# Kernel optimization log

Hardware: AMD Instinct MI355X
Metric: run time of the kernel (lower is better)

## Reference

```python
import jax, jax.numpy as jnp
import numpy as np

B, T, C = 8, 2048, 1024
H, D = 16, 64
DLOW = 64  # D_DECAY = D_AAA = D_MV = D_GATE = 64
EPS_LN = 1e-5


def setup_inputs() -> dict:
    key = jax.random.key(0)
    ks = jax.random.split(key, 26)
    p = lambda k, shape, s=0.02: (jax.random.normal(k, shape, jnp.float32) * s)
    u = lambda k, shape: jax.random.uniform(k, shape, jnp.float32)
    return {
        "x":   jax.random.normal(ks[0], (B, T, C), jnp.float32),
        # token-shift mix coefficients (1,1,C)
        "x_r": u(ks[1], (1, 1, C)), "x_w": u(ks[2], (1, 1, C)),
        "x_k": u(ks[3], (1, 1, C)), "x_v": u(ks[4], (1, 1, C)),
        "x_a": u(ks[5], (1, 1, C)), "x_g": u(ks[6], (1, 1, C)),
        # decay lora: w1 [C,DLOW], w2 [DLOW,H], w0 [1,1,H,1]
        "w0": p(ks[7], (1, 1, H, 1)), "w1": p(ks[8], (C, DLOW)), "w2": p(ks[9], (DLOW, H)),
        # in-context lr lora
        "a0": p(ks[10], (1, 1, H, 1)), "a1": p(ks[11], (C, DLOW)), "a2": p(ks[12], (DLOW, H)),
        # value residual lora
        "v0": p(ks[13], (1, 1, C)), "v1": p(ks[14], (C, DLOW)), "v2": p(ks[15], (DLOW, C)),
        # gate lora
        "g1": p(ks[16], (C, DLOW)), "g2": p(ks[17], (DLOW, C)),
        "k_k": 0.85 + p(ks[18], (1, 1, C)),
        "r_k": p(ks[19], (H, D)),
        # main projections, stored [in, out] so x @ W matches nn.Linear
        "Wr": p(ks[20], (C, C)), "Wk": p(ks[21], (C, C)),
        "Wv": p(ks[22], (C, C)), "Wo": p(ks[23], (C, C)),
        # GroupNorm(n_head, n_embd) affine params
        "ln_w": jnp.ones((C,), jnp.float32) + p(ks[24], (C,)),
        "ln_b": p(ks[25], (C,)),
    }


def reference(x, x_r, x_w, x_k, x_v, x_a, x_g,
              w0, w1, w2, a0, a1, a2, v0, v1, v2, g1, g2,
              k_k, r_k, Wr, Wk, Wv, Wo, ln_w, ln_b):
    Bb, Tt, Cc = x.shape
    Hh, Dd = r_k.shape
    # token shift: sx = x_t - x_{t-1} (zero-padded)
    xx = jnp.concatenate([jnp.zeros((Bb, 1, Cc), x.dtype), x[:, :-1]], axis=1)
    sx = x - xx
    xr = x + sx * x_r
    xw = x + sx * x_w
    xk = x + sx * x_k
    xv = x + sx * x_v
    xa = x + sx * x_a
    xg = x + sx * x_g

    r = (xr @ Wr).reshape(Bb, Tt, Hh, Dd)
    # decay in (0, exp(-0.5)): exp(-softplus(-(w0 + lora)) - 0.5)
    w = jnp.exp(-jax.nn.softplus(-(w0 + (jnp.tanh(xw @ w1) @ w2).reshape(Bb, Tt, Hh, 1))) - 0.5)
    k = xk @ Wk
    v = xv @ Wv
    v_res_gate = jax.nn.sigmoid(v0 + jnp.tanh(xv @ v1) @ v2)
    v = v + (v - v) * v_res_gate  # no-op, kept for faithfulness
    a = jax.nn.sigmoid(a0 + (jnp.tanh(xa @ a1) @ a2).reshape(Bb, Tt, Hh, 1))
    g = jax.nn.sigmoid(jnp.tanh(xg @ g1) @ g2)

    kk = (k * k_k).reshape(Bb, Tt, Hh, Dd)
    kk = kk / jnp.maximum(jnp.linalg.norm(kk, axis=-1, keepdims=True), 1e-12)
    vh = v.reshape(Bb, Tt, Hh, Dd)

    # WKV linear recurrence: state = state * w_t + kk_t * v_t * a_t
    kv = (kk * vh * a).astype(jnp.float32)            # [B,T,H,D]
    w_t = jnp.moveaxis(w.astype(jnp.float32), 1, 0)   # [T,B,H,1]
    kv_t = jnp.moveaxis(kv, 1, 0)                     # [T,B,H,D]

    def step(state, inputs):
        wt, kvt = inputs
        state = state * wt + kvt
        return state, state

    init = jnp.zeros((Bb, Hh, Dd), jnp.float32)
    _, states = jax.lax.scan(step, init, (w_t, kv_t))  # [T,B,H,D]
    x_wkv = jnp.moveaxis(states, 0, 1).astype(x.dtype)  # [B,T,H,D]

    x_wkv = x_wkv * r
    bonus = jnp.sum(r * kk * r_k, axis=-1, keepdims=True) * vh
    x_wkv = x_wkv + bonus  # [B,T,H,D]

    # GroupNorm(H groups over C channels), per (B*T) sample
    mean = x_wkv.mean(axis=-1, keepdims=True)
    var = x_wkv.var(axis=-1, keepdims=True)
    xn = (x_wkv - mean) * jax.lax.rsqrt(var + EPS_LN)
    xn = xn.reshape(Bb, Tt, Cc) * ln_w + ln_b

    return (xn * g) @ Wo
```

## Files before the change

kernel.cpp:

```cpp
#include <hip/hip_runtime.h>


typedef __bf16 bf16;
typedef __attribute__((ext_vector_type(8))) __bf16 bf16x8;
typedef __attribute__((ext_vector_type(4))) float f32x4;

#define TBTOK 16384
#define TSEQ  2048
#define CDIM  1024
#define HN    16
#define CHUNK 32
#define NCH   64

__device__ __forceinline__ float wredsum(float v) {
#pragma unroll
  for (int o = 32; o > 0; o >>= 1) v += __shfl_xor(v, o, 64);
  return v;
}
__device__ __forceinline__ float redsum8(float v) {
#pragma unroll
  for (int o = 4; o > 0; o >>= 1) v += __shfl_xor(v, o, 64);
  return v;
}
__device__ __forceinline__ float sigmf(float x) { return 1.f / (1.f + expf(-x)); }

__device__ __forceinline__ void gl_lds16(const bf16* g, bf16* l) {
  __builtin_amdgcn_global_load_lds(
      (const __attribute__((address_space(1))) unsigned int*)g,
      (__attribute__((address_space(3))) unsigned int*)l, 16, 0, 0);
}

__global__ __launch_bounds__(256) void prep_kern(
    const float* __restrict__ x, const float* __restrict__ mr,
    const float* __restrict__ mk, const float* __restrict__ mv,
    bf16* __restrict__ xr, bf16* __restrict__ xk, bf16* __restrict__ xv,
    bf16* __restrict__ xbf,
    const float* __restrict__ Wr, const float* __restrict__ Wk,
    const float* __restrict__ Wv, const float* __restrict__ Wo,
    const float* __restrict__ w1, const float* __restrict__ a1, const float* __restrict__ g1,
    const float* __restrict__ mw, const float* __restrict__ ma, const float* __restrict__ mg,
    const float* __restrict__ g2, const float* __restrict__ w2, const float* __restrict__ a2,
    bf16* __restrict__ WrT, bf16* __restrict__ WkT, bf16* __restrict__ WvT, bf16* __restrict__ WoT,
    bf16* __restrict__ Bcat, bf16* __restrict__ g2T,
    bf16* __restrict__ w2T, bf16* __restrict__ a2T, float* __restrict__ zpad) {
  int bid0 = blockIdx.x;
  int tid = threadIdx.x;
  if (bid0 < 8192) {
    long i8 = ((long)bid0 * 256 + tid) * 8;
    int m = (int)(i8 >> 10);
    int c = (int)(i8 & 1023);
    f32x4 x0 = *(const f32x4*)(x + i8);
    f32x4 x1 = *(const f32x4*)(x + i8 + 4);
    f32x4 p0 = {0.f, 0.f, 0.f, 0.f}, p1 = {0.f, 0.f, 0.f, 0.f};
    if ((m & (TSEQ - 1)) != 0) {
      p0 = *(const f32x4*)(x + i8 - CDIM);
      p1 = *(const f32x4*)(x + i8 - CDIM + 4);
    }
    f32x4 r0 = *(const f32x4*)(mr + c), r1 = *(const f32x4*)(mr + c + 4);
    f32x4 k0 = *(const f32x4*)(mk + c), k1 = *(const f32x4*)(mk + c + 4);
    f32x4 v0 = *(const f32x4*)(mv + c), v1 = *(const f32x4*)(mv + c + 4);
    bf16x8 or_, ok_, ov_, ox_;
#pragma unroll
    for (int j = 0; j < 4; j++) {
      float s0 = x0[j] - p0[j], s1 = x1[j] - p1[j];
      or_[j] = (bf16)(x0[j] + s0 * r0[j]); or_[4 + j] = (bf16)(x1[j] + s1 * r1[j]);
      ok_[j] = (bf16)(x0[j] + s0 * k0[j]); ok_[4 + j] = (bf16)(x1[j] + s1 * k1[j]);
      ov_[j] = (bf16)(x0[j] + s0 * v0[j]); ov_[4 + j] = (bf16)(x1[j] + s1 * v1[j]);
      ox_[j] = (bf16)x0[j];                ox_[4 + j] = (bf16)x1[j];
    }
    *(bf16x8*)(xr + i8) = or_;
    *(bf16x8*)(xk + i8) = ok_;
    *(bf16x8*)(xv + i8) = ov_;
    *(bf16x8*)(xbf + i8) = ox_;
    return;
  }
  int bid = bid0 - 8192;
  int tx = tid & 31, ty = tid >> 5;
  __shared__ bf16 tile[32][33];
  if (bid < 4096) {
    int sel = bid >> 10, t = bid & 1023;
    int k0 = (t >> 5) * 32, n0 = (t & 31) * 32;
    const float* src = sel == 0 ? Wr : (sel == 1 ? Wk : (sel == 2 ? Wv : Wo));
    bf16* dst = sel == 0 ? WrT : (sel == 1 ? WkT : (sel == 2 ? WvT : WoT));
#pragma unroll
    for (int i = 0; i < 4; i++)
      tile[ty + i * 8][tx] = (bf16)src[(long)(k0 + ty + i * 8) * 1024 + n0 + tx];
    __syncthreads();
#pragma unroll
    for (int i = 0; i < 4; i++)
      dst[(long)(n0 + ty + i * 8) * 1024 + k0 + tx] = tile[tx][ty + i * 8];
  } else if (bid < 4480) {
    int idx = bid - 4096;
    int mat = idx >> 7, rem = idx & 127;
    int half = rem >> 6, t = rem & 63;
    int k0 = (t >> 1) * 32, n0 = (t & 1) * 32;
    const float* W = mat == 0 ? w1 : (mat == 1 ? a1 : g1);
    const float* mx = mat == 0 ? mw : (mat == 1 ? ma : mg);
#pragma unroll
    for (int i = 0; i < 4; i++) {
      int k = k0 + ty + i * 8;
      float s = half == 0 ? (1.f + mx[k]) : (-mx[k]);
      tile[ty + i * 8][tx] = (bf16)(s * W[(long)k * 64 + n0 + tx]);
    }
    __syncthreads();
#pragma unroll
    for (int i = 0; i < 4; i++)
      Bcat[(long)(mat * 64 + n0 + ty + i * 8) * 2048 + half * 1024 + k0 + tx] =
          tile[tx][ty + i * 8];
  } else if (bid < 4544) {
    int t = bid - 4480;
    int k0 = (t >> 5) * 32, n0 = (t & 31) * 32;
#pragma unroll
    for (int i = 0; i < 4; i++)
      tile[ty + i * 8][tx] = (bf16)g2[(long)(k0 + ty + i * 8) * 1024 + n0 + tx];
    __syncthreads();
#pragma unroll
    for (int i = 0; i < 4; i++)
      g2T[(long)(n0 + ty + i * 8) * 64 + k0 + tx] = tile[tx][ty + i * 8];
  } else {
#pragma unroll
    for (int rep = 0; rep < 4; rep++) {
      int idx = rep * 256 + tid;
      int k = idx >> 4, h = idx & 15;
      w2T[h * 64 + k] = (bf16)w2[idx];
      a2T[h * 64 + k] = (bf16)a2[idx];
    }
    if (tid < 64) zpad[tid] = 0.f;
  }
}

template <int ACT, typename OT>
__global__ __launch_bounds__(256) void gemm128_kern(
    const bf16* __restrict__ A0, const bf16* __restrict__ A1, const bf16* __restrict__ A2,
    int apitch,
    const bf16* __restrict__ BT0, const bf16* __restrict__ BT1, const bf16* __restrict__ BT2,
    OT* __restrict__ out0, OT* __restrict__ out1, OT* __restrict__ out2,
    int opitch, int K, int nbpm) {
  int bx = blockIdx.x;
  int mat = bx / nbpm;
  int ncol0 = (bx % nbpm) * 128;
  const bf16* Am = mat == 0 ? A0 : (mat == 1 ? A1 : A2);
  const bf16* BTm = mat == 0 ? BT0 : (mat == 1 ? BT1 : BT2);
  OT* out = mat == 0 ? out0 : (mat == 1 ? out1 : out2);
  int m0 = blockIdx.y * 128;

  __shared__ bf16 Al[128 * 64];
  __shared__ bf16 Bl[128 * 64];

  int tid = threadIdx.x;
  int w = tid >> 6, lane = tid & 63, quad = lane >> 4, lr = lane & 15;
  int wm = (w & 1) * 64, wn = (w >> 1) * 64;

  f32x4 acc[4][4] = {};

  int r0 = tid >> 3;
  int slot = tid & 7;
  int kg = (slot ^ (r0 & 7)) * 8;
  const bf16* ag = Am + (long)(m0 + r0) * apitch + kg;
  const bf16* bg = BTm + (long)(ncol0 + r0) * K + kg;
  long astep = (long)32 * apitch;
  long bstep = (long)32 * K;
  bf16* la = Al + w * 512;
  bf16* lb = Bl + w * 512;

  for (int k0 = 0; k0 < K; k0 += 64) {
#pragma unroll
    for (int s = 0; s < 4; s++) gl_lds16(ag + s * astep, la + s * 2048);
#pragma unroll
    for (int s = 0; s < 4; s++) gl_lds16(bg + s * bstep, lb + s * 2048);
    ag += 64; bg += 64;
    __syncthreads();
#pragma unroll
    for (int ko = 0; ko < 2; ko++) {
      bf16x8 af[4], bff[4];
#pragma unroll
      for (int i = 0; i < 4; i++) {
        int ra = wm + i * 16 + lr;
        af[i] = *(const bf16x8*)&Al[ra * 64 + (((ko * 4 + quad) ^ (ra & 7)) * 8)];
      }
#pragma unroll
      for (int j = 0; j < 4; j++) {
        int rb = wn + j * 16 + lr;
        bff[j] = *(const bf16x8*)&Bl[rb * 64 + (((ko * 4 + quad) ^ (rb & 7)) * 8)];
      }
#pragma unroll
      for (int i = 0; i < 4; i++)
#pragma unroll
        for (int j = 0; j < 4; j++)
          acc[i][j] = __builtin_amdgcn_mfma_f32_16x16x32_bf16(af[i], bff[j], acc[i][j], 0, 0, 0);
    }
    __syncthreads();
  }
#pragma unroll
  for (int i = 0; i < 4; i++)
#pragma unroll
    for (int j = 0; j < 4; j++)
#pragma unroll
      for (int rg = 0; rg < 4; rg++) {
        int row = m0 + wm + i * 16 + quad * 4 + rg;
        int col = ncol0 + wn + j * 16 + lr;
        float v = acc[i][j][rg];
        if (ACT == 1) v = sigmf(v);
        out[(long)row * opitch + col] = (OT)v;
      }
}

__global__ __launch_bounds__(256) void stage1_kern(
    const bf16* __restrict__ xbf, const bf16* __restrict__ Bcat,
    const float* __restrict__ zpad, const bf16* __restrict__ w2T, const bf16* __restrict__ a2T,
    const float* __restrict__ w0, const float* __restrict__ a0,
    bf16* __restrict__ t1g, float* __restrict__ w_arr, float* __restrict__ a_arr) {
  int m0 = blockIdx.x * 64;
  int part = blockIdx.y;
  __shared__ bf16 Al[64 * 32];
  __shared__ bf16 Bl[128 * 32];
  __shared__ bf16 Lt1[64 * 136];

  int tid = threadIdx.x;
  int w = tid >> 6, lane = tid & 63, quad = lane >> 4, lr = lane & 15;
  int wm = w * 16;

  int r0 = tid >> 2, kc0 = (tid & 3) * 8;
  int m = m0 + r0;
  const bf16* asrc = xbf + (long)m * CDIM + kc0;
  bool firstrow = (m & (TSEQ - 1)) == 0;
  const bf16* psrc = firstrow ? (const bf16*)zpad : xbf + (long)(m - 1) * CDIM + kc0;
  int pstep = firstrow ? 0 : 32;
  int brow0 = part ? 128 : 0;
  const bf16* bs0 = Bcat + (long)(brow0 + r0) * 2048 + kc0;
  const bf16* bs1 = bs0 + (long)64 * 2048;
  bf16* la = Al + w * 512;
  bf16* lb0 = Bl + w * 512;
  bf16* lb1 = Bl + 2048 + w * 512;

  if (part == 0) {
    f32x4 acc[8] = {};
#pragma unroll 1
    for (int kk = 0; kk < 64; kk++) {
      if (kk < 32) { gl_lds16(asrc, la); asrc += 32; }
      else         { gl_lds16(psrc, la); psrc += pstep; }
      gl_lds16(bs0, lb0);
      gl_lds16(bs1, lb1);
      bs0 += 32; bs1 += 32;
      __syncthreads();
      bf16x8 af = *(const bf16x8*)&Al[(wm + lr) * 32 + quad * 8];
#pragma unroll
      for (int nf = 0; nf < 8; nf++) {
        bf16x8 bff = *(const bf16x8*)&Bl[(nf * 16 + lr) * 32 + quad * 8];
        acc[nf] = __builtin_amdgcn_mfma_f32_16x16x32_bf16(af, bff, acc[nf], 0, 0, 0);
      }
      __syncthreads();
    }
#pragma unroll
    for (int nf = 0; nf < 8; nf++)
#pragma unroll
      for (int rg = 0; rg < 4; rg++) {
        int row = wm + quad * 4 + rg;
        Lt1[row * 136 + nf * 16 + lr] = (bf16)tanhf(acc[nf][rg]);
      }
    __syncthreads();
#pragma unroll
    for (int rep = 0; rep < 4; rep++) {
      int idx = rep * 256 + tid;
      int row = idx >> 4, h = idx & 15;
      const bf16* rw = &Lt1[row * 136];
      const bf16* ra = rw + 64;
      const bf16* ww = w2T + h * 64;
      const bf16* aw = a2T + h * 64;
      float dw = 0.f, da = 0.f;
#pragma unroll
      for (int k = 0; k < 64; k++) {
        dw += (float)rw[k] * (float)ww[k];
        da += (float)ra[k] * (float)aw[k];
      }
      w_arr[h * TBTOK + m0 + row] = 0.60653066f * sigmf(w0[h] + dw);
      a_arr[h * TBTOK + m0 + row] = sigmf(a0[h] + da);
    }
  } else {
    f32x4 acc[4] = {};
#pragma unroll 1
    for (int kk = 0; kk < 64; kk++) {
      if (kk < 32) { gl_lds16(asrc, la); asrc += 32; }
      else         { gl_lds16(psrc, la); psrc += pstep; }
      gl_lds16(bs0, lb0);
      bs0 += 32;
      __syncthreads();
      bf16x8 af = *(const bf16x8*)&Al[(wm + lr) * 32 + quad * 8];
#pragma unroll
      for (int nf = 0; nf < 4; nf++) {
        bf16x8 bff = *(const bf16x8*)&Bl[(nf * 16 + lr) * 32 + quad * 8];
        acc[nf] = __builtin_amdgcn_mfma_f32_16x16x32_bf16(af, bff, acc[nf], 0, 0, 0);
      }
      __syncthreads();
    }
#pragma unroll
    for (int nf = 0; nf < 4; nf++)
#pragma unroll
      for (int rg = 0; rg < 4; rg++) {
        int row = wm + quad * 4 + rg;
        t1g[(long)(m0 + row) * 64 + nf * 16 + lr] = (bf16)tanhf(acc[nf][rg]);
      }
  }
}

__global__ __launch_bounds__(256) void scan1_kern(
    const bf16* __restrict__ k_buf, const bf16* __restrict__ v_buf, const bf16* __restrict__ r_buf,
    const float* __restrict__ k_k, const float* __restrict__ r_k,
    const float* __restrict__ a_arr, const float* __restrict__ w_arr,
    float* __restrict__ kv2, float* __restrict__ Parr, float* __restrict__ bonus,
    float* __restrict__ Lend) {
  int wid = blockIdx.x * 4 + (threadIdx.x >> 6);
  int lane = threadIdx.x & 63;
  int bh = wid >> 6, c = wid & 63;
  int b = bh >> 4, h = bh & 15;
  int mstart = b * TSEQ + c * CHUNK;
  int kc = h * 64 + lane;
  float kkc = k_k[kc], rkc = r_k[kc];
  float st = 0.f, cw = 1.f;
  long mbase = (long)mstart * CDIM + kc;
  int hm = h * TBTOK + mstart;
  long sbase = ((long)hm) * 64 + lane;
  float kf = (float)k_buf[mbase] * kkc;
  float vf = (float)v_buf[mbase];
  float rf = (float)r_buf[mbase];
  float af = a_arr[hm];
  float wt = w_arr[hm];
  for (int t = 0; t < CHUNK; t++) {
    float kf_n = 0.f, vf_n = 0.f, rf_n = 0.f, af_n = 0.f, wt_n = 0.f;
    if (t < CHUNK - 1) {
      kf_n = (float)k_buf[mbase + CDIM] * kkc;
      vf_n = (float)v_buf[mbase + CDIM];
      rf_n = (float)r_buf[mbase + CDIM];
      af_n = a_arr[hm + 1];
      wt_n = w_arr[hm + 1];
    }
    float ss = wredsum(kf * kf);
    float kkn = kf / fmaxf(sqrtf(ss), 1e-12f);
    st = st * wt + kkn * vf * af;
    kv2[sbase] = st;
    cw *= wt;
    float bs = wredsum(rf * kkn * rkc);
    if (lane == 0) {
      Parr[hm] = cw;
      bonus[(mstart + t) * HN + h] = bs;
    }
    kf = kf_n; vf = vf_n; rf = rf_n; af = af_n; wt = wt_n;
    mbase += CDIM; hm += 1; sbase += 64;
  }
  Lend[(long)wid * 64 + lane] = st;
}

__global__ __launch_bounds__(256) void gate_post_kern(
    const bf16* __restrict__ t1g, const bf16* __restrict__ g2T,
    const float* __restrict__ kv2, const float* __restrict__ Parr,
    const float* __restrict__ Lend, const float* __restrict__ bonus,
    bf16* __restrict__ r_buf, const bf16* __restrict__ v_buf,
    const float* __restrict__ ln_w, const float* __restrict__ ln_b) {
  int ncol0 = blockIdx.x * 128;
  int m0 = blockIdx.y * 128;

  __shared__ bf16 Al[128 * 32];
  __shared__ bf16 Bl[128 * 32];
  __shared__ bf16 gtile[128 * 136];

  int tid = threadIdx.x;
  int w = tid >> 6, lane = tid & 63, quad = lane >> 4, lr = lane & 15;
  int wm = (w & 1) * 64, wn = (w >> 1) * 64;

  f32x4 acc[4][4] = {};

  int r0 = tid >> 2, kc0 = (tid & 3) * 8;
  const bf16* ag0 = t1g + (long)(m0 + r0) * 64 + kc0;
  const bf16* ag1 = ag0 + (long)64 * 64;
  const bf16* bg0 = g2T + (long)(ncol0 + r0) * 64 + kc0;
  const bf16* bg1 = bg0 + (long)64 * 64;
  bf16* la0 = Al + w * 512;
  bf16* la1 = Al + 2048 + w * 512;
  bf16* lb0 = Bl + w * 512;
  bf16* lb1 = Bl + 2048 + w * 512;

  for (int k0 = 0; k0 < 64; k0 += 32) {
    gl_lds16(ag0, la0);
    gl_lds16(ag1, la1);
    gl_lds16(bg0, lb0);
    gl_lds16(bg1, lb1);
    ag0 += 32; ag1 += 32; bg0 += 32; bg1 += 32;
    __syncthreads();
    bf16x8 af[4], bff[4];
#pragma unroll
    for (int i = 0; i < 4; i++) af[i] = *(const bf16x8*)&Al[(wm + i * 16 + lr) * 32 + quad * 8];
#pragma unroll
    for (int j = 0; j < 4; j++) bff[j] = *(const bf16x8*)&Bl[(wn + j * 16 + lr) * 32 + quad * 8];
#pragma unroll
    for (int i = 0; i < 4; i++)
#pragma unroll
      for (int j = 0; j < 4; j++)
        acc[i][j] = __builtin_amdgcn_mfma_f32_16x16x32_bf16(af[i], bff[j], acc[i][j], 0, 0, 0);
    __syncthreads();
  }
#pragma unroll
  for (int i = 0; i < 4; i++)
#pragma unroll
    for (int j = 0; j < 4; j++)
#pragma unroll
      for (int rg = 0; rg < 4; rg++) {
        int row = wm + i * 16 + quad * 4 + rg;
        int col = wn + j * 16 + lr;
        gtile[row * 136 + col] = (bf16)sigmf(acc[i][j][rg]);
      }
  __syncthreads();

  int c_loc = (tid & 15) * 8;
  int col_g = ncol0 + c_loc;
  int h = col_g >> 6;
  int d0 = col_g & 63;
  f32x4 lnw0 = *(const f32x4*)(ln_w + col_g);
  f32x4 lnw1 = *(const f32x4*)(ln_w + col_g + 4);
  f32x4 lnb0 = *(const f32x4*)(ln_b + col_g);
  f32x4 lnb1 = *(const f32x4*)(ln_b + col_g + 4);
#pragma unroll
  for (int jj = 0; jj < 8; jj++) {
    int row = jj * 16 + (tid >> 4);
    int row_g = m0 + row;
    int b = row_g >> 11;
    int ch = (row_g & (TSEQ - 1)) >> 5;
    long kvb = ((long)h * TBTOK + row_g) * 64 + d0;
    f32x4 st0 = *(const f32x4*)(kv2 + kvb);
    f32x4 st1 = *(const f32x4*)(kv2 + kvb + 4);
    f32x4 cy0 = {0.f, 0.f, 0.f, 0.f}, cy1 = {0.f, 0.f, 0.f, 0.f};
    if (ch != 0) {
      long lb = ((long)((b * 16 + h) * NCH + ch - 1)) * 64 + d0;
      cy0 = *(const f32x4*)(Lend + lb);
      cy1 = *(const f32x4*)(Lend + lb + 4);
    }
    float pw = Parr[h * TBTOK + row_g];
    float bs = bonus[row_g * HN + h];
    long rb = (long)row_g * CDIM + col_g;
    bf16x8 rf8 = *(const bf16x8*)(r_buf + rb);
    bf16x8 vf8 = *(const bf16x8*)(v_buf + rb);
    bf16x8 g8 = *(const bf16x8*)&gtile[row * 136 + c_loc];
    float xw[8];
#pragma unroll
    for (int q = 0; q < 4; q++) {
      xw[q]     = (st0[q] + pw * cy0[q]) * (float)rf8[q]     + bs * (float)vf8[q];
      xw[4 + q] = (st1[q] + pw * cy1[q]) * (float)rf8[4 + q] + bs * (float)vf8[4 + q];
    }
    float sum = 0.f;
#pragma unroll
    for (int q = 0; q < 8; q++) sum += xw[q];
    float mn = redsum8(sum) * (1.f / 64.f);
    float vs = 0.f;
#pragma unroll
    for (int q = 0; q < 8; q++) {
      xw[q] -= mn;
      vs += xw[q] * xw[q];
    }
    float var = redsum8(vs) * (1.f / 64.f);
    float rq = rsqrtf(var + 1e-5f);
    bf16x8 o8;
#pragma unroll
    for (int q = 0; q < 4; q++) {
      o8[q]     = (bf16)((xw[q] * rq * lnw0[q] + lnb0[q]) * (float)g8[q]);
      o8[4 + q] = (bf16)((xw[4 + q] * rq * lnw1[q] + lnb1[q]) * (float)g8[4 + q]);
    }
    *(bf16x8*)(r_buf + rb) = o8;
  }
}

extern "C" void kernel_launch(void* const* d_in, const int* in_sizes, int n_in,
                              void* d_out, int out_size, void* d_ws, size_t ws_size,
                              hipStream_t stream) {
  const float* x    = (const float*)d_in[0];
  const float* x_r  = (const float*)d_in[1];
  const float* x_w  = (const float*)d_in[2];
  const float* x_k  = (const float*)d_in[3];
  const float* x_v  = (const float*)d_in[4];
  const float* x_a  = (const float*)d_in[5];
  const float* x_g  = (const float*)d_in[6];
  const float* w0   = (const float*)d_in[7];
  const float* w1   = (const float*)d_in[8];
  const float* w2   = (const float*)d_in[9];
  const float* a0   = (const float*)d_in[10];
  const float* a1   = (const float*)d_in[11];
  const float* a2   = (const float*)d_in[12];
  const float* g1   = (const float*)d_in[16];
  const float* g2   = (const float*)d_in[17];
  const float* k_k  = (const float*)d_in[18];
  const float* r_k  = (const float*)d_in[19];
  const float* Wr   = (const float*)d_in[20];
  const float* Wk   = (const float*)d_in[21];
  const float* Wv   = (const float*)d_in[22];
  const float* Wo   = (const float*)d_in[23];
  const float* ln_w = (const float*)d_in[24];
  const float* ln_b = (const float*)d_in[25];
  float* out = (float*)d_out;

  char* p = (char*)d_ws;
  auto carve = [&](size_t bytes) {
    void* r = (void*)p;
    p += (bytes + 255) & ~(size_t)255;
    return r;
  };
  bf16* WrT = (bf16*)carve(1024 * 1024 * 2);
  bf16* WkT = (bf16*)carve(1024 * 1024 * 2);
  bf16* WvT = (bf16*)carve(1024 * 1024 * 2);
  bf16* WoT = (bf16*)carve(1024 * 1024 * 2);
  bf16* Bcat = (bf16*)carve(192 * 2048 * 2);
  bf16* g2T  = (bf16*)carve(1024 * 64 * 2);
  bf16* w2T  = (bf16*)carve(16 * 64 * 2);
  bf16* a2T  = (bf16*)carve(16 * 64 * 2);
  float* zpad = (float*)carve(64 * 4);
  bf16* t1g   = (bf16*)carve((size_t)TBTOK * 64 * 2);
  bf16* r_buf = (bf16*)carve((size_t)TBTOK * CDIM * 2);
  bf16* k_buf = (bf16*)carve((size_t)TBTOK * CDIM * 2);
  bf16* v_buf = (bf16*)carve((size_t)TBTOK * CDIM * 2);
  float* w_arr = (float*)carve((size_t)TBTOK * HN * 4);
  float* a_arr = (float*)carve((size_t)TBTOK * HN * 4);
  float* bonus = (float*)carve((size_t)TBTOK * HN * 4);
  float* Parr  = (float*)carve((size_t)TBTOK * HN * 4);
  float* Lend  = (float*)carve((size_t)128 * NCH * 64 * 4);
  bf16* xr  = (bf16*)carve((size_t)TBTOK * CDIM * 2);
  bf16* xk  = (bf16*)carve((size_t)TBTOK * CDIM * 2);
  bf16* xv  = (bf16*)carve((size_t)TBTOK * CDIM * 2);
  bf16* xbf = (bf16*)carve((size_t)TBTOK * CDIM * 2);
  float* kv2 = (float*)xv;

  prep_kern<<<dim3(8192 + 4545), 256, 0, stream>>>(
      x, x_r, x_k, x_v, xr, xk, xv, xbf,
      Wr, Wk, Wv, Wo, w1, a1, g1, x_w, x_a, x_g, g2, w2, a2,
      WrT, WkT, WvT, WoT, Bcat, g2T, w2T, a2T, zpad);
  stage1_kern<<<dim3(TBTOK / 64, 2), 256, 0, stream>>>(
      xbf, Bcat, zpad, w2T, a2T, w0, a0, t1g, w_arr, a_arr);
  gemm128_kern<0, bf16><<<dim3(24, TBTOK / 128), 256, 0, stream>>>(
      xr, xk, xv, CDIM, WrT, WkT, WvT,
      r_buf, k_buf, v_buf, CDIM, 1024, 8);
  scan1_kern<<<dim3(128 * NCH / 4), 256, 0, stream>>>(
      k_buf, v_buf, r_buf, k_k, r_k, a_arr, w_arr, kv2, Parr, bonus, Lend);
  gate_post_kern<<<dim3(8, TBTOK / 128), 256, 0, stream>>>(
      t1g, g2T, kv2, Parr, Lend, bonus, r_buf, v_buf, ln_w, ln_b);
  gemm128_kern<0, float><<<dim3(8, TBTOK / 128), 256, 0, stream>>>(
      r_buf, r_buf, r_buf, CDIM, WoT, WoT, WoT,
      out, out, out, CDIM, 1024, 8);
}
```

Before: 572.2 us.

## Replace 128x128 GEMM with double-buffered 256x256 tile GEMM and XCD-aware block remap

Rewrites the projection GEMM kernel to use 256x256 output tiles with 512 threads, double-buffered LDS staging with explicit vmcnt waits, and MFMA issue at raised priority. Block IDs are remapped so consecutive tiles land on the same XCD, improving L2 reuse. The larger tiles cut global reloads of A and B per FLOP, but they raise register and LDS pressure and leave fewer blocks for the output GEMM (256 blocks).

```diff
diff --git a/kernel.cpp b/kernel.cpp
--- a/kernel.cpp
+++ b/kernel.cpp
@@ -129,79 +129,130 @@
   }
 }
 
-template <int ACT, typename OT>
-__global__ __launch_bounds__(256) void gemm128_kern(
+template <typename OT>
+__global__ __launch_bounds__(512, 2) void gemm256_kern(
     const bf16* __restrict__ A0, const bf16* __restrict__ A1, const bf16* __restrict__ A2,
-    int apitch,
     const bf16* __restrict__ BT0, const bf16* __restrict__ BT1, const bf16* __restrict__ BT2,
     OT* __restrict__ out0, OT* __restrict__ out1, OT* __restrict__ out2,
-    int opitch, int K, int nbpm) {
-  int bx = blockIdx.x;
-  int mat = bx / nbpm;
-  int ncol0 = (bx % nbpm) * 128;
+    int K, int nbpm) {
+  int nwg = gridDim.x;
+  int id = blockIdx.x;
+  int qq = nwg >> 3;
+  int wg = (id & 7) * qq + (id >> 3);
+  int mat = wg / nbpm;
+  int rem = wg - mat * nbpm;
+  int m0 = (rem & 63) << 8;
+  int n0 = (rem >> 6) << 8;
   const bf16* Am = mat == 0 ? A0 : (mat == 1 ? A1 : A2);
   const bf16* BTm = mat == 0 ? BT0 : (mat == 1 ? BT1 : BT2);
   OT* out = mat == 0 ? out0 : (mat == 1 ? out1 : out2);
-  int m0 = blockIdx.y * 128;
-
-  __shared__ bf16 Al[128 * 64];
-  __shared__ bf16 Bl[128 * 64];
+
+  __shared__ bf16 Al[2][256 * 64];
+  __shared__ bf16 Bl[2][256 * 64];
 
   int tid = threadIdx.x;
   int w = tid >> 6, lane = tid & 63, quad = lane >> 4, lr = lane & 15;
-  int wm = (w & 1) * 64, wn = (w >> 1) * 64;
-
-  f32x4 acc[4][4] = {};
-
-  int r0 = tid >> 3;
-  int slot = tid & 7;
+  int wr = w >> 2, wc = w & 3;
+
+  int r0 = tid >> 3, slot = tid & 7;
   int kg = (slot ^ (r0 & 7)) * 8;
-  const bf16* ag = Am + (long)(m0 + r0) * apitch + kg;
-  const bf16* bg = BTm + (long)(ncol0 + r0) * K + kg;
-  long astep = (long)32 * apitch;
-  long bstep = (long)32 * K;
-  bf16* la = Al + w * 512;
-  bf16* lb = Bl + w * 512;
-
-  for (int k0 = 0; k0 < K; k0 += 64) {
-#pragma unroll
-    for (int s = 0; s < 4; s++) gl_lds16(ag + s * astep, la + s * 2048);
-#pragma unroll
-    for (int s = 0; s < 4; s++) gl_lds16(bg + s * bstep, lb + s * 2048);
-    ag += 64; bg += 64;
-    __syncthreads();
-#pragma unroll
-    for (int ko = 0; ko < 2; ko++) {
-      bf16x8 af[4], bff[4];
-#pragma unroll
-      for (int i = 0; i < 4; i++) {
-        int ra = wm + i * 16 + lr;
-        af[i] = *(const bf16x8*)&Al[ra * 64 + (((ko * 4 + quad) ^ (ra & 7)) * 8)];
-      }
-#pragma unroll
-      for (int j = 0; j < 4; j++) {
-        int rb = wn + j * 16 + lr;
-        bff[j] = *(const bf16x8*)&Bl[rb * 64 + (((ko * 4 + quad) ^ (rb & 7)) * 8)];
-      }
+  const bf16* ag = Am + (long)(m0 + r0) * K + kg;
+  const bf16* bg = BTm + (long)(n0 + r0) * K + kg;
+  long rstep = (long)64 * K;
+  bf16* laW = &Al[0][0] + w * 512;
+  bf16* lbW = &Bl[0][0] + w * 512;
+
+  auto stage = [&](int bsel, int t) {
+    const bf16* a = ag + t * 64;
+    const bf16* b = bg + t * 64;
+    bf16* la = laW + bsel * 16384;
+    bf16* lb = lbW + bsel * 16384;
+#pragma unroll
+    for (int s = 0; s < 4; s++) gl_lds16(a + s * rstep, la + s * 4096);
+#pragma unroll
+    for (int s = 0; s < 4; s++) gl_lds16(b + s * rstep, lb + s * 4096);
+  };
+
+  f32x4 acc[8][4] = {};
+  stage(0, 0);
+  stage(1, 1);
+  asm volatile("s_waitcnt vmcnt(8)" ::: "memory");
+  __builtin_amdgcn_s_barrier();
+
+  int NT = K >> 6;
+#pragma unroll 1
+  for (int t = 0; t < NT; t++) {
+    int cur = t & 1;
+    const bf16* Ab = &Al[0][0] + cur * 16384;
+    const bf16* Bb = &Bl[0][0] + cur * 16384;
+    bf16x8 af[4][2], bfr[4][2];
+#pragma unroll
+    for (int j = 0; j < 4; j++) {
+      int rb = wc * 64 + j * 16 + lr;
+#pragma unroll
+      for (int ks = 0; ks < 2; ks++)
+        bfr[j][ks] = *(const bf16x8*)&Bb[rb * 64 + (((ks * 4 + quad) ^ (rb & 7)) * 8)];
+    }
+#pragma unroll
+    for (int i = 0; i < 4; i++) {
+      int ra = wr * 128 + i * 16 + lr;
+#pragma unroll
+      for (int ks = 0; ks < 2; ks++)
+        af[i][ks] = *(const bf16x8*)&Ab[ra * 64 + (((ks * 4 + quad) ^ (ra & 7)) * 8)];
+    }
+    __builtin_amdgcn_s_barrier();
+    asm volatile("s_waitcnt lgkmcnt(0)" ::: "memory");
+    __builtin_amdgcn_sched_barrier(0);
+    __builtin_amdgcn_s_setprio(1);
+#pragma unroll
+    for (int ks = 0; ks < 2; ks++)
 #pragma unroll
       for (int i = 0; i < 4; i++)
 #pragma unroll
         for (int j = 0; j < 4; j++)
-          acc[i][j] = __builtin_amdgcn_mfma_f32_16x16x32_bf16(af[i], bff[j], acc[i][j], 0, 0, 0);
-    }
-    __syncthreads();
-  }
-#pragma unroll
-  for (int i = 0; i < 4; i++)
+          acc[i][j] =
+              __builtin_amdgcn_mfma_f32_16x16x32_bf16(af[i][ks], bfr[j][ks], acc[i][j], 0, 0, 0);
+    __builtin_amdgcn_s_setprio(0);
+    __builtin_amdgcn_s_barrier();
+#pragma unroll
+    for (int i = 0; i < 4; i++) {
+      int ra = wr * 128 + 64 + i * 16 + lr;
+#pragma unroll
+      for (int ks = 0; ks < 2; ks++)
+        af[i][ks] = *(const bf16x8*)&Ab[ra * 64 + (((ks * 4 + quad) ^ (ra & 7)) * 8)];
+    }
+    __builtin_amdgcn_s_barrier();
+    asm volatile("s_waitcnt lgkmcnt(0)" ::: "memory");
+    __builtin_amdgcn_sched_barrier(0);
+    __builtin_amdgcn_s_setprio(1);
+#pragma unroll
+    for (int ks = 0; ks < 2; ks++)
+#pragma unroll
+      for (int i = 0; i < 4; i++)
+#pragma unroll
+        for (int j = 0; j < 4; j++)
+          acc[4 + i][j] = __builtin_amdgcn_mfma_f32_16x16x32_bf16(af[i][ks], bfr[j][ks],
+                                                                  acc[4 + i][j], 0, 0, 0);
+    __builtin_amdgcn_s_setprio(0);
+    __builtin_amdgcn_s_barrier();
+    if (t + 2 < NT) {
+      stage(cur, t + 2);
+      asm volatile("s_waitcnt vmcnt(8)" ::: "memory");
+    } else {
+      asm volatile("s_waitcnt vmcnt(0)" ::: "memory");
+    }
+    __builtin_amdgcn_s_barrier();
+  }
+
+#pragma unroll
+  for (int i = 0; i < 8; i++)
 #pragma unroll
     for (int j = 0; j < 4; j++)
 #pragma unroll
       for (int rg = 0; rg < 4; rg++) {
-        int row = m0 + wm + i * 16 + quad * 4 + rg;
-        int col = ncol0 + wn + j * 16 + lr;
-        float v = acc[i][j][rg];
-        if (ACT == 1) v = sigmf(v);
-        out[(long)row * opitch + col] = (OT)v;
+        int row = m0 + wr * 128 + i * 16 + quad * 4 + rg;
+        int col = n0 + wc * 64 + j * 16 + lr;
+        out[(long)row * CDIM + col] = (OT)acc[i][j][rg];
       }
 }
 
@@ -531,14 +582,12 @@
       WrT, WkT, WvT, WoT, Bcat, g2T, w2T, a2T, zpad);
   stage1_kern<<<dim3(TBTOK / 64, 2), 256, 0, stream>>>(
       xbf, Bcat, zpad, w2T, a2T, w0, a0, t1g, w_arr, a_arr);
-  gemm128_kern<0, bf16><<<dim3(24, TBTOK / 128), 256, 0, stream>>>(
-      xr, xk, xv, CDIM, WrT, WkT, WvT,
-      r_buf, k_buf, v_buf, CDIM, 1024, 8);
+  gemm256_kern<bf16><<<dim3(768), 512, 0, stream>>>(
+      xr, xk, xv, WrT, WkT, WvT, r_buf, k_buf, v_buf, 1024, 256);
   scan1_kern<<<dim3(128 * NCH / 4), 256, 0, stream>>>(
       k_buf, v_buf, r_buf, k_k, r_k, a_arr, w_arr, kv2, Parr, bonus, Lend);
   gate_post_kern<<<dim3(8, TBTOK / 128), 256, 0, stream>>>(
       t1g, g2T, kv2, Parr, Lend, bonus, r_buf, v_buf, ln_w, ln_b);
-  gemm128_kern<0, float><<<dim3(8, TBTOK / 128), 256, 0, stream>>>(
-      r_buf, r_buf, r_buf, CDIM, WoT, WoT, WoT,
-      out, out, out, CDIM, 1024, 8);
-}
+  gemm256_kern<float><<<dim3(256), 512, 0, stream>>>(
+      r_buf, r_buf, r_buf, WoT, WoT, WoT, out, out, out, 1024, 256);
+}
```

Result: faster. 548.5 us (-4.1%).
